# Performance work log

Measured on AMD Instinct MI355X. Metric: run time of the kernel, lower is better.

Reference implementation:

```python
import jax, jax.numpy as jnp
import numpy as np

B, D, H, E, C, TOPK = 16384, 2048, 2048, 6, 1024, 3

def setup_inputs() -> dict:
    key = jax.random.key(0)
    ks = jax.random.split(key, 8)
    s_d = 1.0 / np.sqrt(D)
    s_h = 1.0 / np.sqrt(H)
    return {
        "x": jax.random.normal(ks[0], (B, D), dtype=jnp.float32),
        "gate_W": jax.random.uniform(ks[1], (E, D), jnp.float32, -s_d, s_d),
        "gate_b": jax.random.uniform(ks[2], (E,), jnp.float32, -s_d, s_d),
        "W1": jax.random.uniform(ks[3], (E, H, D), jnp.float32, -s_d, s_d),
        "b1": jax.random.uniform(ks[4], (E, H), jnp.float32, -s_d, s_d),
        "W2": jax.random.uniform(ks[5], (E, C, H), jnp.float32, -s_h, s_h),
        "b2": jax.random.uniform(ks[6], (E, C), jnp.float32, -s_h, s_h),
    }

def reference(x, gate_W, gate_b, W1, b1, W2, b2):
    # gating: top-k sparse softmax
    gate_logits = x @ gate_W.T + gate_b                      # [B, E]
    topk_vals, topk_idx = jax.lax.top_k(gate_logits, TOPK)   # [B, K]
    neg_inf = jnp.finfo(gate_logits.dtype).min
    sparse = jnp.full_like(gate_logits, neg_inf)
    rows = jnp.arange(gate_logits.shape[0])[:, None]
    sparse = sparse.at[rows, topk_idx].set(topk_vals)
    gw = jax.nn.softmax(sparse, axis=-1)                     # [B, E]
    # dense experts: Linear -> GELU (exact, erf) -> Linear (dropout is eval no-op)
    h = jnp.einsum('bd,ehd->beh', x, W1) + b1[None]          # [B, E, H]
    h = jax.nn.gelu(h, approximate=False)
    expert_outs = jnp.einsum('beh,ech->bec', h, W2) + b2[None]  # [B, E, C]
    out = jnp.einsum('be,bec->bc', gw, expert_outs)          # masked combine
    return (out, gw)
```

## Files before the change

### kernel.cpp

```cpp
#include <hip/hip_runtime.h>
#include <hip/hip_bf16.h>
#include <math.h>

#define B_ 16384
#define D_ 2048
#define H_ 2048
#define E_ 6
#define C_ 1024

typedef __attribute__((ext_vector_type(8))) short short8;
typedef __attribute__((ext_vector_type(4))) float f32x4;

__device__ __forceinline__ unsigned short f2bf(float f) {
    __hip_bfloat16 h = __float2bfloat16(f);
    return *reinterpret_cast<unsigned short*>(&h);
}

__device__ __forceinline__ void async_copy16(const unsigned short* g, unsigned short* l) {
    __builtin_amdgcn_global_load_lds(
        (const __attribute__((address_space(1))) unsigned int*)(g),
        (__attribute__((address_space(3))) unsigned int*)(l), 16, 0, 0);
}

__global__ void gate_kernel(const float* __restrict__ x, const float* __restrict__ gW,
                            const float* __restrict__ gb, float* __restrict__ gw_out,
                            int* __restrict__ counts, int* __restrict__ rowlist,
                            float* __restrict__ wtslist) {
    int wave = threadIdx.x >> 6;
    int lane = threadIdx.x & 63;
    int row  = blockIdx.x * 4 + wave;
    const float* xr = x + (size_t)row * D_;
    double acc[E_] = {0, 0, 0, 0, 0, 0};
    for (int i = 0; i < D_ / 64; ++i) {
        int d = i * 64 + lane;
        double xv = (double)xr[d];
#pragma unroll
        for (int e = 0; e < E_; ++e) acc[e] += xv * (double)gW[e * D_ + d];
    }
#pragma unroll
    for (int off = 32; off > 0; off >>= 1) {
#pragma unroll
        for (int e = 0; e < E_; ++e) acc[e] += __shfl_down(acc[e], off);
    }
    if (lane == 0) {
        double lg[E_];
#pragma unroll
        for (int e = 0; e < E_; ++e) lg[e] = acc[e] + (double)gb[e];
        bool used[E_] = {false, false, false, false, false, false};
        int idx[3]; double val[3];
        for (int k = 0; k < 3; ++k) {
            int best = -1; double bv = -1e300;
            for (int e = 0; e < E_; ++e)
                if (!used[e] && lg[e] > bv) { bv = lg[e]; best = e; }
            used[best] = true; idx[k] = best; val[k] = bv;
        }
        double m = val[0];
        double w[3]; double s = 0.0;
        for (int k = 0; k < 3; ++k) { w[k] = exp(val[k] - m); s += w[k]; }
        float gwv[E_] = {0.f, 0.f, 0.f, 0.f, 0.f, 0.f};
        for (int k = 0; k < 3; ++k) gwv[idx[k]] = (float)(w[k] / s);
#pragma unroll
        for (int e = 0; e < E_; ++e) gw_out[(size_t)row * E_ + e] = gwv[e];
        for (int k = 0; k < 3; ++k) {
            int e = idx[k];
            int pos = atomicAdd(&counts[e], 1);
            rowlist[(size_t)e * B_ + pos] = row * 3 + k;
            wtslist[(size_t)e * B_ + pos] = (float)(w[k] / s);
        }
    }
}

__global__ void cast_f32_bf16(const float* __restrict__ in, unsigned short* __restrict__ out, int n4) {
    int i = blockIdx.x * blockDim.x + threadIdx.x;
    if (i < n4) {
        float4 v = ((const float4*)in)[i];
        ushort4 u;
        u.x = f2bf(v.x); u.y = f2bf(v.y); u.z = f2bf(v.z); u.w = f2bf(v.w);
        ((ushort4*)out)[i] = u;
    }
}


#define GEMM_PROLOGUE_AND_LOOP(KDIM)                                                     \
    int lane = tid & 63;                                                                 \
    int wv   = tid >> 6;                                                                 \
    int wrow = (wv >> 1) * 64;                                                           \
    int wcol = (wv & 1) * 64;                                                            \
    int fm   = lane & 15;                                                                \
    int kg   = lane >> 4;                                                                \
    int fsw  = fm & 7;                                                                   \
    f32x4 acc[4][4] = {};                                                                \
    unsigned short* A0 = As;                unsigned short* Bq0 = Bs;                    \
    unsigned short* A1 = As + 256 * 64;     unsigned short* Bq1 = Bs + 128 * 64;         \
    unsigned short* A2 = As + 2 * 256 * 64; unsigned short* Bq2 = Bs + 2 * 128 * 64;     \
    _Pragma("unroll")                                                                    \
    for (int it = 0; it < 4; ++it) async_copy16(aptr[it], A0 + (it * 512 + tid) * 8);    \
    _Pragma("unroll")                                                                    \
    for (int it = 0; it < 2; ++it) async_copy16(bptr[it], Bq0 + (it * 512 + tid) * 8);   \
    _Pragma("unroll")                                                                    \
    for (int it = 0; it < 4; ++it) async_copy16(aptr[it] + 64, A1 + (it * 512 + tid) * 8); \
    _Pragma("unroll")                                                                    \
    for (int it = 0; it < 2; ++it) async_copy16(bptr[it] + 64, Bq1 + (it * 512 + tid) * 8); \
    asm volatile("s_waitcnt vmcnt(6)" ::: "memory");                                     \
    __builtin_amdgcn_s_barrier();                                                        \
    __builtin_amdgcn_sched_barrier(0);                                                   \
    const int NT = (KDIM) / 64;                                                          \
    for (int t = 0; t < NT; ++t) {                                                       \
        const bool st  = (t + 2 < NT);                                                   \
        const int  k0s = (t + 2) * 64;                                                   \
        {                                              \
            short8 aF[4], bF[4];                                                         \
            int go = (kg ^ fsw) * 8;                                                     \
            _Pragma("unroll")                                                            \
            for (int mi = 0; mi < 4; ++mi)                                               \
                aF[mi] = *(const short8*)(A0 + (wrow + mi * 16 + fm) * 64 + go);         \
            _Pragma("unroll")                                                            \
            for (int ni = 0; ni < 4; ++ni)                                               \
                bF[ni] = *(const short8*)(Bq0 + (wcol + ni * 16 + fm) * 64 + go);        \
            if (st) {                                                                    \
                async_copy16(aptr[0] + k0s, A2 + (0 * 512 + tid) * 8);                   \
                async_copy16(aptr[1] + k0s, A2 + (1 * 512 + tid) * 8);                   \
                async_copy16(bptr[0] + k0s, Bq2 + (0 * 512 + tid) * 8);                  \
            }                                                                            \
            __builtin_amdgcn_s_barrier();                                                \
            asm volatile("s_waitcnt lgkmcnt(0)" ::: "memory");                           \
            __builtin_amdgcn_sched_barrier(0);                                           \
            __builtin_amdgcn_s_setprio(1);                                               \
            _Pragma("unroll")                                                            \
            for (int mi = 0; mi < 4; ++mi)                                               \
                _Pragma("unroll")                                                        \
                for (int ni = 0; ni < 4; ++ni)                                           \
                    acc[mi][ni] = __builtin_amdgcn_mfma_f32_16x16x32_bf16(               \
                        aF[mi], bF[ni], acc[mi][ni], 0, 0, 0);                           \
            __builtin_amdgcn_s_setprio(0);                                               \
            __builtin_amdgcn_s_barrier();                                                \
            __builtin_amdgcn_sched_barrier(0);                                           \
        }                                                                                \
        {                                              \
            short8 aF[4], bF[4];                                                         \
            int go = ((4 + kg) ^ fsw) * 8;                                               \
            _Pragma("unroll")                                                            \
            for (int mi = 0; mi < 4; ++mi)                                               \
                aF[mi] = *(const short8*)(A0 + (wrow + mi * 16 + fm) * 64 + go);         \
            _Pragma("unroll")                                                            \
            for (int ni = 0; ni < 4; ++ni)                                               \
                bF[ni] = *(const short8*)(Bq0 + (wcol + ni * 16 + fm) * 64 + go);        \
            if (st) {                                                                    \
                async_copy16(aptr[2] + k0s, A2 + (2 * 512 + tid) * 8);                   \
                async_copy16(aptr[3] + k0s, A2 + (3 * 512 + tid) * 8);                   \
                async_copy16(bptr[1] + k0s, Bq2 + (1 * 512 + tid) * 8);                  \
            }                                                                            \
            __builtin_amdgcn_s_barrier();                                                \
            asm volatile("s_waitcnt lgkmcnt(0)" ::: "memory");                           \
            __builtin_amdgcn_sched_barrier(0);                                           \
            __builtin_amdgcn_s_setprio(1);                                               \
            _Pragma("unroll")                                                            \
            for (int mi = 0; mi < 4; ++mi)                                               \
                _Pragma("unroll")                                                        \
                for (int ni = 0; ni < 4; ++ni)                                           \
                    acc[mi][ni] = __builtin_amdgcn_mfma_f32_16x16x32_bf16(               \
                        aF[mi], bF[ni], acc[mi][ni], 0, 0, 0);                           \
            __builtin_amdgcn_s_setprio(0);                                               \
        }                                                                                \
           \
        if (st) asm volatile("s_waitcnt vmcnt(6)" ::: "memory");                         \
        else    asm volatile("s_waitcnt vmcnt(0)" ::: "memory");                         \
        __builtin_amdgcn_s_barrier();                                                    \
        __builtin_amdgcn_sched_barrier(0);                                               \
        unsigned short* tA = A0; A0 = A1; A1 = A2; A2 = tA;                              \
        unsigned short* tB = Bq0; Bq0 = Bq1; Bq1 = Bq2; Bq2 = tB;                        \
    }

__global__ __launch_bounds__(512, 2) void gemm1_kernel(
    const unsigned short* __restrict__ xb, const unsigned short* __restrict__ W1b,
    const float* __restrict__ b1, const int* __restrict__ counts,
    const int* __restrict__ rowlist, unsigned short* __restrict__ hbuf) {
    int e = blockIdx.z;
    int cnt = counts[e];
    int m0 = blockIdx.y * 256;
    if (m0 >= cnt) return;
    int n0 = blockIdx.x * 128;

    __shared__ __align__(16) unsigned short As[3 * 256 * 64];
    __shared__ __align__(16) unsigned short Bs[3 * 128 * 64];

    int tid = threadIdx.x;
    const int* rlist = rowlist + (size_t)e * B_;

    const unsigned short* aptr[4];
    const unsigned short* bptr[2];
#pragma unroll
    for (int it = 0; it < 4; ++it) {
        int seg = it * 512 + tid;
        int r = seg >> 3, c = seg & 7;
        int cs = c ^ (r & 7);
        int idx = m0 + r; if (idx >= cnt) idx = cnt - 1;
        aptr[it] = xb + (size_t)(rlist[idx] / 3) * D_ + cs * 8;
    }
#pragma unroll
    for (int it = 0; it < 2; ++it) {
        int seg = it * 512 + tid;
        int r = seg >> 3, c = seg & 7;
        int cs = c ^ (r & 7);
        bptr[it] = W1b + (size_t)e * H_ * D_ + (size_t)(n0 + r) * D_ + cs * 8;
    }

    GEMM_PROLOGUE_AND_LOOP(D_)

    int rlim = cnt - m0;
#pragma unroll
    for (int mi = 0; mi < 4; ++mi) {
#pragma unroll
        for (int i = 0; i < 4; ++i) {
            int r = wrow + mi * 16 + kg * 4 + i;
            if (r < rlim) {
                size_t base = (size_t)rlist[m0 + r] * H_ + n0;
#pragma unroll
                for (int ni = 0; ni < 4; ++ni) {
                    int col = wcol + ni * 16 + fm;
                    float v = acc[mi][ni][i] + b1[e * H_ + n0 + col];
                    v = 0.5f * v * (1.0f + erff(v * 0.70710678118654752f));
                    hbuf[base + col] = f2bf(v);
                }
            }
        }
    }
}

__global__ __launch_bounds__(512, 2) void gemm2_kernel(
    const unsigned short* __restrict__ hbuf, const unsigned short* __restrict__ W2b,
    const float* __restrict__ b2, const int* __restrict__ counts,
    const int* __restrict__ rowlist, const float* __restrict__ wtslist,
    float* __restrict__ sbuf, float* __restrict__ out) {
    int e = blockIdx.z;
    int cnt = counts[e];
    int m0 = blockIdx.y * 256;
    if (m0 >= cnt) return;
    int n0 = blockIdx.x * 128;

    __shared__ __align__(16) unsigned short As[3 * 256 * 64];
    __shared__ __align__(16) unsigned short Bs[3 * 128 * 64];

    int tid = threadIdx.x;
    const int* rlist = rowlist + (size_t)e * B_;
    const float* wlist = wtslist + (size_t)e * B_;

    const unsigned short* aptr[4];
    const unsigned short* bptr[2];
#pragma unroll
    for (int it = 0; it < 4; ++it) {
        int seg = it * 512 + tid;
        int r = seg >> 3, c = seg & 7;
        int cs = c ^ (r & 7);
        int idx = m0 + r; if (idx >= cnt) idx = cnt - 1;
        aptr[it] = hbuf + (size_t)rlist[idx] * H_ + cs * 8;
    }
#pragma unroll
    for (int it = 0; it < 2; ++it) {
        int seg = it * 512 + tid;
        int r = seg >> 3, c = seg & 7;
        int cs = c ^ (r & 7);
        bptr[it] = W2b + (size_t)e * C_ * H_ + (size_t)(n0 + r) * H_ + cs * 8;
    }

    GEMM_PROLOGUE_AND_LOOP(H_)

    int rlim = cnt - m0;
#pragma unroll
    for (int mi = 0; mi < 4; ++mi) {
#pragma unroll
        for (int i = 0; i < 4; ++i) {
            int r = wrow + mi * 16 + kg * 4 + i;
            if (r < rlim) {
                int slot = rlist[m0 + r];
                float w  = wlist[m0 + r];
                if (sbuf) {
                    float* srow = sbuf + (size_t)slot * C_ + n0;
#pragma unroll
                    for (int ni = 0; ni < 4; ++ni) {
                        int col = wcol + ni * 16 + fm;
                        srow[col] = (acc[mi][ni][i] + b2[e * C_ + n0 + col]) * w;
                    }
                } else {
                    float* orow = out + (size_t)(slot / 3) * C_ + n0;
#pragma unroll
                    for (int ni = 0; ni < 4; ++ni) {
                        int col = wcol + ni * 16 + fm;
                        atomicAdd(&orow[col], (acc[mi][ni][i] + b2[e * C_ + n0 + col]) * w);
                    }
                }
            }
        }
    }
}

__global__ void combine_kernel(const float* __restrict__ sbuf, float* __restrict__ out) {
    int i   = blockIdx.x * 256 + threadIdx.x;
    int row = i >> 8;
    int c4  = i & 255;
    const float4* s4 = (const float4*)sbuf;
    size_t b = (size_t)row * 3 * 256 + c4;
    float4 a = s4[b], d = s4[b + 256], g = s4[b + 512];
    float4 r;
    r.x = a.x + d.x + g.x; r.y = a.y + d.y + g.y;
    r.z = a.z + d.z + g.z; r.w = a.w + d.w + g.w;
    ((float4*)out)[i] = r;
}

extern "C" void kernel_launch(void* const* d_in, const int* in_sizes, int n_in,
                              void* d_out, int out_size, void* d_ws, size_t ws_size,
                              hipStream_t stream) {
    const float* x  = (const float*)d_in[0];
    const float* gW = (const float*)d_in[1];
    const float* gb = (const float*)d_in[2];
    const float* W1 = (const float*)d_in[3];
    const float* b1 = (const float*)d_in[4];
    const float* W2 = (const float*)d_in[5];
    const float* b2 = (const float*)d_in[6];
    float* out    = (float*)d_out;
    float* gw_out = out + (size_t)B_ * C_;

    char* ws = (char*)d_ws;
    size_t off = 0;
    auto alloc = [&](size_t bytes) -> char* {
        char* p = ws + off;
        off = (off + bytes + 255) & ~(size_t)255;
        return p;
    };
    int*            counts  = (int*)alloc(E_ * 4);
    int*            rowlist = (int*)alloc((size_t)E_ * B_ * 4);
    float*          wtslist = (float*)alloc((size_t)E_ * B_ * 4);
    unsigned short* xb      = (unsigned short*)alloc((size_t)B_ * D_ * 2);
    unsigned short* W1b     = (unsigned short*)alloc((size_t)E_ * H_ * D_ * 2);
    unsigned short* W2b     = (unsigned short*)alloc((size_t)E_ * C_ * H_ * 2);
    unsigned short* hbuf    = (unsigned short*)alloc((size_t)3 * B_ * H_ * 2);
    float*          sbuf    = (float*)alloc((size_t)3 * B_ * C_ * 4);
    bool use_sbuf = (ws_size == 0) || (off <= ws_size);
    (void)in_sizes; (void)n_in; (void)out_size;

    hipMemsetAsync(counts, 0, E_ * 4, stream);
    if (!use_sbuf) hipMemsetAsync(out, 0, (size_t)B_ * C_ * 4, stream);

    gate_kernel<<<B_ / 4, 256, 0, stream>>>(x, gW, gb, gw_out, counts, rowlist, wtslist);
    cast_f32_bf16<<<(B_ * D_ / 4) / 256, 256, 0, stream>>>(x, xb, B_ * D_ / 4);
    cast_f32_bf16<<<(E_ * H_ * D_ / 4) / 256, 256, 0, stream>>>(W1, W1b, E_ * H_ * D_ / 4);
    cast_f32_bf16<<<(E_ * C_ * H_ / 4) / 256, 256, 0, stream>>>(W2, W2b, E_ * C_ * H_ / 4);
    gemm1_kernel<<<dim3(H_ / 128, B_ / 256, E_), 512, 0, stream>>>(xb, W1b, b1, counts, rowlist, hbuf);
    gemm2_kernel<<<dim3(C_ / 128, B_ / 256, E_), 512, 0, stream>>>(hbuf, W2b, b2, counts, rowlist, wtslist,
                                                                   use_sbuf ? sbuf : (float*)nullptr, out);
    if (use_sbuf)
        combine_kernel<<<(B_ * C_ / 4) / 256, 256, 0, stream>>>(sbuf, out);
}
```

Measured before the change: 2.088 ms.

## Enlarge GEMM tiles to 256x256 with 4-stage K32 pipeline and grouped block order

Replaces the 256x128 tile, K64 triple-buffered GEMM core with a 256x256 tile, K32 four-stage async LDS pipeline. Each wave now owns a 128x64 sub-tile, which raises MFMA work per LDS fragment load. Blocks are remapped so groups of 8 row tiles share column tiles, for better L2 reuse. It also fuses the x-to-bf16 cast into the gate kernel and lets sbuf alias the xb/W1b workspace region. In exchange it uses 128 accumulator registers per thread and puts occupancy at risk under launch_bounds(512,2).

```diff
diff --git a/kernel.cpp b/kernel.cpp
--- a/kernel.cpp
+++ b/kernel.cpp
@@ -25,15 +25,18 @@
 __global__ void gate_kernel(const float* __restrict__ x, const float* __restrict__ gW,
                             const float* __restrict__ gb, float* __restrict__ gw_out,
                             int* __restrict__ counts, int* __restrict__ rowlist,
-                            float* __restrict__ wtslist) {
+                            float* __restrict__ wtslist, unsigned short* __restrict__ xb) {
     int wave = threadIdx.x >> 6;
     int lane = threadIdx.x & 63;
     int row  = blockIdx.x * 4 + wave;
     const float* xr = x + (size_t)row * D_;
+    unsigned short* xbr = xb + (size_t)row * D_;
     double acc[E_] = {0, 0, 0, 0, 0, 0};
     for (int i = 0; i < D_ / 64; ++i) {
         int d = i * 64 + lane;
-        double xv = (double)xr[d];
+        float xf = xr[d];
+        xbr[d] = f2bf(xf);
+        double xv = (double)xf;
 #pragma unroll
         for (int e = 0; e < E_; ++e) acc[e] += xv * (double)gW[e * D_ + d];
     }
@@ -81,95 +84,67 @@
 }
 
 
-#define GEMM_PROLOGUE_AND_LOOP(KDIM)                                                     \
-    int lane = tid & 63;                                                                 \
-    int wv   = tid >> 6;                                                                 \
-    int wrow = (wv >> 1) * 64;                                                           \
-    int wcol = (wv & 1) * 64;                                                            \
-    int fm   = lane & 15;                                                                \
-    int kg   = lane >> 4;                                                                \
-    int fsw  = fm & 7;                                                                   \
-    f32x4 acc[4][4] = {};                                                                \
-    unsigned short* A0 = As;                unsigned short* Bq0 = Bs;                    \
-    unsigned short* A1 = As + 256 * 64;     unsigned short* Bq1 = Bs + 128 * 64;         \
-    unsigned short* A2 = As + 2 * 256 * 64; unsigned short* Bq2 = Bs + 2 * 128 * 64;     \
-    _Pragma("unroll")                                                                    \
-    for (int it = 0; it < 4; ++it) async_copy16(aptr[it], A0 + (it * 512 + tid) * 8);    \
-    _Pragma("unroll")                                                                    \
-    for (int it = 0; it < 2; ++it) async_copy16(bptr[it], Bq0 + (it * 512 + tid) * 8);   \
-    _Pragma("unroll")                                                                    \
-    for (int it = 0; it < 4; ++it) async_copy16(aptr[it] + 64, A1 + (it * 512 + tid) * 8); \
-    _Pragma("unroll")                                                                    \
-    for (int it = 0; it < 2; ++it) async_copy16(bptr[it] + 64, Bq1 + (it * 512 + tid) * 8); \
-    asm volatile("s_waitcnt vmcnt(6)" ::: "memory");                                     \
-    __builtin_amdgcn_s_barrier();                                                        \
-    __builtin_amdgcn_sched_barrier(0);                                                   \
-    const int NT = (KDIM) / 64;                                                          \
-    for (int t = 0; t < NT; ++t) {                                                       \
-        const bool st  = (t + 2 < NT);                                                   \
-        const int  k0s = (t + 2) * 64;                                                   \
-        {                                              \
-            short8 aF[4], bF[4];                                                         \
-            int go = (kg ^ fsw) * 8;                                                     \
-            _Pragma("unroll")                                                            \
-            for (int mi = 0; mi < 4; ++mi)                                               \
-                aF[mi] = *(const short8*)(A0 + (wrow + mi * 16 + fm) * 64 + go);         \
-            _Pragma("unroll")                                                            \
-            for (int ni = 0; ni < 4; ++ni)                                               \
-                bF[ni] = *(const short8*)(Bq0 + (wcol + ni * 16 + fm) * 64 + go);        \
-            if (st) {                                                                    \
-                async_copy16(aptr[0] + k0s, A2 + (0 * 512 + tid) * 8);                   \
-                async_copy16(aptr[1] + k0s, A2 + (1 * 512 + tid) * 8);                   \
-                async_copy16(bptr[0] + k0s, Bq2 + (0 * 512 + tid) * 8);                  \
-            }                                                                            \
-            __builtin_amdgcn_s_barrier();                                                \
-            asm volatile("s_waitcnt lgkmcnt(0)" ::: "memory");                           \
-            __builtin_amdgcn_sched_barrier(0);                                           \
-            __builtin_amdgcn_s_setprio(1);                                               \
-            _Pragma("unroll")                                                            \
-            for (int mi = 0; mi < 4; ++mi)                                               \
-                _Pragma("unroll")                                                        \
-                for (int ni = 0; ni < 4; ++ni)                                           \
-                    acc[mi][ni] = __builtin_amdgcn_mfma_f32_16x16x32_bf16(               \
-                        aF[mi], bF[ni], acc[mi][ni], 0, 0, 0);                           \
-            __builtin_amdgcn_s_setprio(0);                                               \
-            __builtin_amdgcn_s_barrier();                                                \
-            __builtin_amdgcn_sched_barrier(0);                                           \
-        }                                                                                \
-        {                                              \
-            short8 aF[4], bF[4];                                                         \
-            int go = ((4 + kg) ^ fsw) * 8;                                               \
-            _Pragma("unroll")                                                            \
-            for (int mi = 0; mi < 4; ++mi)                                               \
-                aF[mi] = *(const short8*)(A0 + (wrow + mi * 16 + fm) * 64 + go);         \
-            _Pragma("unroll")                                                            \
-            for (int ni = 0; ni < 4; ++ni)                                               \
-                bF[ni] = *(const short8*)(Bq0 + (wcol + ni * 16 + fm) * 64 + go);        \
-            if (st) {                                                                    \
-                async_copy16(aptr[2] + k0s, A2 + (2 * 512 + tid) * 8);                   \
-                async_copy16(aptr[3] + k0s, A2 + (3 * 512 + tid) * 8);                   \
-                async_copy16(bptr[1] + k0s, Bq2 + (1 * 512 + tid) * 8);                  \
-            }                                                                            \
-            __builtin_amdgcn_s_barrier();                                                \
-            asm volatile("s_waitcnt lgkmcnt(0)" ::: "memory");                           \
-            __builtin_amdgcn_sched_barrier(0);                                           \
-            __builtin_amdgcn_s_setprio(1);                                               \
-            _Pragma("unroll")                                                            \
-            for (int mi = 0; mi < 4; ++mi)                                               \
-                _Pragma("unroll")                                                        \
-                for (int ni = 0; ni < 4; ++ni)                                           \
-                    acc[mi][ni] = __builtin_amdgcn_mfma_f32_16x16x32_bf16(               \
-                        aF[mi], bF[ni], acc[mi][ni], 0, 0, 0);                           \
-            __builtin_amdgcn_s_setprio(0);                                               \
-        }                                                                                \
-           \
-        if (st) asm volatile("s_waitcnt vmcnt(6)" ::: "memory");                         \
-        else    asm volatile("s_waitcnt vmcnt(0)" ::: "memory");                         \
-        __builtin_amdgcn_s_barrier();                                                    \
-        __builtin_amdgcn_sched_barrier(0);                                               \
-        unsigned short* tA = A0; A0 = A1; A1 = A2; A2 = tA;                              \
-        unsigned short* tB = Bq0; Bq0 = Bq1; Bq1 = Bq2; Bq2 = tB;                        \
-    }
+#define GEMM_CORE(KDIM)                                                          \
+    int lane = tid & 63;                                                         \
+    int wv   = tid >> 6;                                                         \
+    int wr   = wv >> 2;                                       \
+    int wc   = wv & 3;                                      \
+    int fm   = lane & 15;                                                        \
+    int kg   = lane >> 4;                                                        \
+    int laneoff = ((fm >> 1) << 6) + ((((fm & 1) << 2) + kg) ^ ((fm >> 1) & 7)) * 8; \
+    int aBase = wr * 4096 + laneoff;                                             \
+    int bBase = wc * 2048 + laneoff;                                             \
+    f32x4 acc[8][4] = {};                                                        \
+    const int NT = (KDIM) / 32;                                                  \
+    _Pragma("unroll")                                                            \
+    for (int pt = 0; pt < 3; ++pt) {                                             \
+        unsigned short* Ab = As + pt * 8192;                                     \
+        unsigned short* Bb = Bs + pt * 8192;                                     \
+        int k0 = pt * 32;                                                        \
+        async_copy16(aptr[0] + k0, Ab + (0 * 512 + tid) * 8);                    \
+        async_copy16(aptr[1] + k0, Ab + (1 * 512 + tid) * 8);                    \
+        async_copy16(bptr[0] + k0, Bb + (0 * 512 + tid) * 8);                    \
+        async_copy16(bptr[1] + k0, Bb + (1 * 512 + tid) * 8);                    \
+    }                                                                            \
+    asm volatile("s_waitcnt vmcnt(8)" ::: "memory");                             \
+    __builtin_amdgcn_s_barrier();                                                \
+    __builtin_amdgcn_sched_barrier(0);                                           \
+    for (int t = 0; t < NT; ++t) {                                               \
+        unsigned short* Ab = As + (t & 3) * 8192;                                \
+        unsigned short* Bb = Bs + (t & 3) * 8192;                                \
+        if (t + 3 < NT) {                                                        \
+            unsigned short* An = As + ((t + 3) & 3) * 8192;                      \
+            unsigned short* Bn = Bs + ((t + 3) & 3) * 8192;                      \
+            int k0 = (t + 3) * 32;                                               \
+            async_copy16(aptr[0] + k0, An + (0 * 512 + tid) * 8);                \
+            async_copy16(aptr[1] + k0, An + (1 * 512 + tid) * 8);                \
+            async_copy16(bptr[0] + k0, Bn + (0 * 512 + tid) * 8);                \
+            async_copy16(bptr[1] + k0, Bn + (1 * 512 + tid) * 8);                \
+        }                                                                        \
+        short8 bF[4];                                                            \
+        _Pragma("unroll")                                                        \
+        for (int n = 0; n < 4; ++n)                                              \
+            bF[n] = *(const short8*)(Bb + bBase + n * 512);                      \
+        _Pragma("unroll")                                                        \
+        for (int m = 0; m < 8; ++m) {                                            \
+            short8 aF = *(const short8*)(Ab + aBase + m * 512);                  \
+            _Pragma("unroll")                                                    \
+            for (int n = 0; n < 4; ++n)                                          \
+                acc[m][n] = __builtin_amdgcn_mfma_f32_16x16x32_bf16(             \
+                    aF, bF[n], acc[m][n], 0, 0, 0);                              \
+        }                                                                        \
+        if (t + 3 < NT)      asm volatile("s_waitcnt vmcnt(8)" ::: "memory");    \
+        else if (t + 2 < NT) asm volatile("s_waitcnt vmcnt(4)" ::: "memory");    \
+        else                 asm volatile("s_waitcnt vmcnt(0)" ::: "memory");    \
+        __builtin_amdgcn_s_barrier();                                            \
+        __builtin_amdgcn_sched_barrier(0);                                       \
+    }
+
+#define SLOT_DECODE(s, R, g)                                                     \
+    int rr_##R = (s) >> 3;                                                       \
+    int pp_##R = ((s) & 7) ^ (rr_##R & 7);                                       \
+    int R = 2 * rr_##R + (pp_##R >> 2);                                          \
+    int g = pp_##R & 3;
 
 __global__ __launch_bounds__(512, 2) void gemm1_kernel(
     const unsigned short* __restrict__ xb, const unsigned short* __restrict__ W1b,
@@ -177,48 +152,43 @@
     const int* __restrict__ rowlist, unsigned short* __restrict__ hbuf) {
     int e = blockIdx.z;
     int cnt = counts[e];
-    int m0 = blockIdx.y * 256;
+    int flat = blockIdx.x;
+    int p  = (flat & 7) + ((flat >> 6) << 3);
+    int nb = (flat >> 3) & 7;
+    int m0 = p * 256;
     if (m0 >= cnt) return;
-    int n0 = blockIdx.x * 128;
-
-    __shared__ __align__(16) unsigned short As[3 * 256 * 64];
-    __shared__ __align__(16) unsigned short Bs[3 * 128 * 64];
-
+    int n0 = nb * 256;
+
+    __shared__ __align__(16) unsigned short As[4 * 8192];
+    __shared__ __align__(16) unsigned short Bs[4 * 8192];
     int tid = threadIdx.x;
     const int* rlist = rowlist + (size_t)e * B_;
 
-    const unsigned short* aptr[4];
+    const unsigned short* aptr[2];
     const unsigned short* bptr[2];
 #pragma unroll
-    for (int it = 0; it < 4; ++it) {
-        int seg = it * 512 + tid;
-        int r = seg >> 3, c = seg & 7;
-        int cs = c ^ (r & 7);
-        int idx = m0 + r; if (idx >= cnt) idx = cnt - 1;
-        aptr[it] = xb + (size_t)(rlist[idx] / 3) * D_ + cs * 8;
-    }
-#pragma unroll
     for (int it = 0; it < 2; ++it) {
-        int seg = it * 512 + tid;
-        int r = seg >> 3, c = seg & 7;
-        int cs = c ^ (r & 7);
-        bptr[it] = W1b + (size_t)e * H_ * D_ + (size_t)(n0 + r) * D_ + cs * 8;
-    }
-
-    GEMM_PROLOGUE_AND_LOOP(D_)
+        int s = it * 512 + tid;
+        SLOT_DECODE(s, Ra, ga)
+        int idx = m0 + Ra; if (idx >= cnt) idx = cnt - 1;
+        aptr[it] = xb + (size_t)(rlist[idx] / 3) * D_ + ga * 8;
+        bptr[it] = W1b + (size_t)e * H_ * D_ + (size_t)(n0 + Ra) * D_ + ga * 8;
+    }
+
+    GEMM_CORE(D_)
 
     int rlim = cnt - m0;
 #pragma unroll
-    for (int mi = 0; mi < 4; ++mi) {
+    for (int m = 0; m < 8; ++m) {
 #pragma unroll
         for (int i = 0; i < 4; ++i) {
-            int r = wrow + mi * 16 + kg * 4 + i;
+            int r = wr * 128 + m * 16 + kg * 4 + i;
             if (r < rlim) {
                 size_t base = (size_t)rlist[m0 + r] * H_ + n0;
 #pragma unroll
-                for (int ni = 0; ni < 4; ++ni) {
-                    int col = wcol + ni * 16 + fm;
-                    float v = acc[mi][ni][i] + b1[e * H_ + n0 + col];
+                for (int n = 0; n < 4; ++n) {
+                    int col = wc * 64 + n * 16 + fm;
+                    float v = acc[m][n][i] + b1[e * H_ + n0 + col];
                     v = 0.5f * v * (1.0f + erff(v * 0.70710678118654752f));
                     hbuf[base + col] = f2bf(v);
                 }
@@ -234,59 +204,54 @@
     float* __restrict__ sbuf, float* __restrict__ out) {
     int e = blockIdx.z;
     int cnt = counts[e];
-    int m0 = blockIdx.y * 256;
+    int flat = blockIdx.x;
+    int p  = (flat & 7) + ((flat >> 5) << 3);
+    int nb = (flat >> 3) & 3;
+    int m0 = p * 256;
     if (m0 >= cnt) return;
-    int n0 = blockIdx.x * 128;
-
-    __shared__ __align__(16) unsigned short As[3 * 256 * 64];
-    __shared__ __align__(16) unsigned short Bs[3 * 128 * 64];
-
+    int n0 = nb * 256;
+
+    __shared__ __align__(16) unsigned short As[4 * 8192];
+    __shared__ __align__(16) unsigned short Bs[4 * 8192];
     int tid = threadIdx.x;
     const int* rlist = rowlist + (size_t)e * B_;
     const float* wlist = wtslist + (size_t)e * B_;
 
-    const unsigned short* aptr[4];
+    const unsigned short* aptr[2];
     const unsigned short* bptr[2];
 #pragma unroll
-    for (int it = 0; it < 4; ++it) {
-        int seg = it * 512 + tid;
-        int r = seg >> 3, c = seg & 7;
-        int cs = c ^ (r & 7);
-        int idx = m0 + r; if (idx >= cnt) idx = cnt - 1;
-        aptr[it] = hbuf + (size_t)rlist[idx] * H_ + cs * 8;
-    }
-#pragma unroll
     for (int it = 0; it < 2; ++it) {
-        int seg = it * 512 + tid;
-        int r = seg >> 3, c = seg & 7;
-        int cs = c ^ (r & 7);
-        bptr[it] = W2b + (size_t)e * C_ * H_ + (size_t)(n0 + r) * H_ + cs * 8;
-    }
-
-    GEMM_PROLOGUE_AND_LOOP(H_)
+        int s = it * 512 + tid;
+        SLOT_DECODE(s, Ra, ga)
+        int idx = m0 + Ra; if (idx >= cnt) idx = cnt - 1;
+        aptr[it] = hbuf + (size_t)rlist[idx] * H_ + ga * 8;
+        bptr[it] = W2b + (size_t)e * C_ * H_ + (size_t)(n0 + Ra) * H_ + ga * 8;
+    }
+
+    GEMM_CORE(H_)
 
     int rlim = cnt - m0;
 #pragma unroll
-    for (int mi = 0; mi < 4; ++mi) {
+    for (int m = 0; m < 8; ++m) {
 #pragma unroll
         for (int i = 0; i < 4; ++i) {
-            int r = wrow + mi * 16 + kg * 4 + i;
+            int r = wr * 128 + m * 16 + kg * 4 + i;
             if (r < rlim) {
                 int slot = rlist[m0 + r];
                 float w  = wlist[m0 + r];
                 if (sbuf) {
                     float* srow = sbuf + (size_t)slot * C_ + n0;
 #pragma unroll
-                    for (int ni = 0; ni < 4; ++ni) {
-                        int col = wcol + ni * 16 + fm;
-                        srow[col] = (acc[mi][ni][i] + b2[e * C_ + n0 + col]) * w;
+                    for (int n = 0; n < 4; ++n) {
+                        int col = wc * 64 + n * 16 + fm;
+                        srow[col] = (acc[m][n][i] + b2[e * C_ + n0 + col]) * w;
                     }
                 } else {
                     float* orow = out + (size_t)(slot / 3) * C_ + n0;
 #pragma unroll
-                    for (int ni = 0; ni < 4; ++ni) {
-                        int col = wcol + ni * 16 + fm;
-                        atomicAdd(&orow[col], (acc[mi][ni][i] + b2[e * C_ + n0 + col]) * w);
+                    for (int n = 0; n < 4; ++n) {
+                        int col = wc * 64 + n * 16 + fm;
+                        atomicAdd(&orow[col], (acc[m][n][i] + b2[e * C_ + n0 + col]) * w);
                     }
                 }
             }
@@ -330,24 +295,25 @@
     int*            counts  = (int*)alloc(E_ * 4);
     int*            rowlist = (int*)alloc((size_t)E_ * B_ * 4);
     float*          wtslist = (float*)alloc((size_t)E_ * B_ * 4);
+    unsigned short* W2b     = (unsigned short*)alloc((size_t)E_ * C_ * H_ * 2);
+    unsigned short* hbuf    = (unsigned short*)alloc((size_t)3 * B_ * H_ * 2);
+    size_t region_off = off;
     unsigned short* xb      = (unsigned short*)alloc((size_t)B_ * D_ * 2);
     unsigned short* W1b     = (unsigned short*)alloc((size_t)E_ * H_ * D_ * 2);
-    unsigned short* W2b     = (unsigned short*)alloc((size_t)E_ * C_ * H_ * 2);
-    unsigned short* hbuf    = (unsigned short*)alloc((size_t)3 * B_ * H_ * 2);
-    float*          sbuf    = (float*)alloc((size_t)3 * B_ * C_ * 4);
-    bool use_sbuf = (ws_size == 0) || (off <= ws_size);
+    float*          sbuf    = (float*)(ws + region_off);
+    size_t sbuf_end = region_off + (size_t)3 * B_ * C_ * 4;
+    bool use_sbuf = (ws_size == 0) || (sbuf_end <= ws_size);
     (void)in_sizes; (void)n_in; (void)out_size;
 
     hipMemsetAsync(counts, 0, E_ * 4, stream);
     if (!use_sbuf) hipMemsetAsync(out, 0, (size_t)B_ * C_ * 4, stream);
 
-    gate_kernel<<<B_ / 4, 256, 0, stream>>>(x, gW, gb, gw_out, counts, rowlist, wtslist);
-    cast_f32_bf16<<<(B_ * D_ / 4) / 256, 256, 0, stream>>>(x, xb, B_ * D_ / 4);
+    gate_kernel<<<B_ / 4, 256, 0, stream>>>(x, gW, gb, gw_out, counts, rowlist, wtslist, xb);
     cast_f32_bf16<<<(E_ * H_ * D_ / 4) / 256, 256, 0, stream>>>(W1, W1b, E_ * H_ * D_ / 4);
     cast_f32_bf16<<<(E_ * C_ * H_ / 4) / 256, 256, 0, stream>>>(W2, W2b, E_ * C_ * H_ / 4);
-    gemm1_kernel<<<dim3(H_ / 128, B_ / 256, E_), 512, 0, stream>>>(xb, W1b, b1, counts, rowlist, hbuf);
-    gemm2_kernel<<<dim3(C_ / 128, B_ / 256, E_), 512, 0, stream>>>(hbuf, W2b, b2, counts, rowlist, wtslist,
-                                                                   use_sbuf ? sbuf : (float*)nullptr, out);
+    gemm1_kernel<<<dim3(8 * (B_ / 256), 1, E_), 512, 0, stream>>>(xb, W1b, b1, counts, rowlist, hbuf);
+    gemm2_kernel<<<dim3(4 * (B_ / 256), 1, E_), 512, 0, stream>>>(hbuf, W2b, b2, counts, rowlist, wtslist,
+                                                                  use_sbuf ? sbuf : (float*)nullptr, out);
     if (use_sbuf)
         combine_kernel<<<(B_ * C_ / 4) / 256, 256, 0, stream>>>(sbuf, out);
 }
```

Measured after the change: 2.050 ms. About the same (-1.8%).
